# Optimization experiments

Hardware: AMD Instinct MI355X
Metric: run time of the kernel (lower is better)

The kernel has to match this reference:

```python
import jax, jax.numpy as jnp
import numpy as np

N, D, H = 4096, 1024, 16
HD = D // H  # 64
EPS = 1e-5


def setup_inputs() -> dict:
    key = jax.random.key(0)
    ks = jax.random.split(key, 12)
    lim = 1.0 / np.sqrt(D)
    def lin(kw, kb):
        W = jax.random.uniform(kw, (D, D), jnp.float32, -lim, lim)
        b = jax.random.uniform(kb, (D,), jnp.float32, -lim, lim)
        return W, b
    Wq, bq = lin(ks[0], ks[1])
    Wk, bk = lin(ks[2], ks[3])
    Wv, bv = lin(ks[4], ks[5])
    Wo, bo = lin(ks[6], ks[7])
    return {
        "query": jax.random.normal(ks[8], (N, D), jnp.float32),
        "key": jax.random.normal(ks[9], (N, D), jnp.float32),
        "value": jax.random.normal(ks[10], (N, D), jnp.float32),
        "Wq": Wq, "bq": bq, "Wk": Wk, "bk": bk,
        "Wv": Wv, "bv": bv, "Wo": Wo, "bo": bo,
        "q_norm_w": jnp.ones((HD,), jnp.float32),
        "k_norm_w": jnp.ones((HD,), jnp.float32),
    }


def _rmsnorm(x, w):
    # eqx.nn.RMSNorm: weight-only, eps=1e-5, over last dim
    inv = jax.lax.rsqrt(jnp.mean(x * x, axis=-1, keepdims=True) + EPS)
    return w * x * inv


def reference(query, key, value, Wq, bq, Wk, bk, Wv, bv, Wo, bo, q_norm_w, k_norm_w):
    n = query.shape[0]
    q = (query @ Wq.T + bq).reshape(n, H, HD)
    k = (key @ Wk.T + bk).reshape(n, H, HD)
    v = (value @ Wv.T + bv).reshape(n, H, HD)
    q = _rmsnorm(q, q_norm_w)
    k = _rmsnorm(k, k_norm_w)
    # scale=1.0: raw unscaled dot-product logits
    logits = jnp.einsum('qhd,khd->hqk', q, k)  # [H, N, N]
    probs = jax.nn.softmax(logits, axis=-1)
    attn = jnp.einsum('hqk,khd->qhd', probs, v).reshape(n, H * HD)
    return attn @ Wo.T + bo
```

## Files before the change

### kernel.cpp

```cpp
#include <hip/hip_runtime.h>
#include <stdint.h>
#include <stddef.h>

#define N_TOK 4096
#define DM    1024
#define NHEAD 16
#define HD    64

typedef __attribute__((ext_vector_type(8)))  short bf16x8;
typedef __attribute__((ext_vector_type(4)))  short bf16x4;
typedef __attribute__((ext_vector_type(4)))  float f32x4;
typedef __attribute__((ext_vector_type(16))) float f32x16;

static __device__ __forceinline__ float bf2f(short u) {
  union { unsigned int i; float f; } c;
  c.i = ((unsigned int)(unsigned short)u) << 16;
  return c.f;
}
static __device__ __forceinline__ unsigned short f2bf(float f) {
  union { float f; unsigned int i; } c; c.f = f;
  unsigned int x = c.i;
  return (unsigned short)((x + 0x7fffu + ((x >> 16) & 1u)) >> 16);
}
static __device__ __forceinline__ unsigned int cvtpk(float lo, float hi) {
  unsigned int d;
  asm("v_cvt_pk_bf16_f32 %0, %1, %2" : "=v"(d) : "v"(lo), "v"(hi));
  return d;
}
static __device__ __forceinline__ void plswap(unsigned int& a, unsigned int& b) {
  asm("v_permlane32_swap_b32 %0, %1" : "+v"(a), "+v"(b));
}
#if __has_builtin(__builtin_amdgcn_exp2f)
#define EXP2(x) __builtin_amdgcn_exp2f(x)
#else
#define EXP2(x) exp2f(x)
#endif
static __device__ __forceinline__ void gload16(const void* g, void* l) {
  __builtin_amdgcn_global_load_lds(
      (const __attribute__((address_space(1))) unsigned int*)g,
      (__attribute__((address_space(3))) unsigned int*)l, 16, 0, 0);
}

struct Cvt7 { const float* s[7]; unsigned short* d[7]; };
__global__ void cvt_all(Cvt7 a) {
  int u0 = blockIdx.x << 10;
  int seg, off;
  if (u0 < 1572864) { seg = u0 >> 19; off = u0 & 524287; }
  else { int j = u0 - 1572864; seg = 3 + (j >> 17); off = j & 131071; }
  const float* s = a.s[seg];
  unsigned short* dd = a.d[seg];
  int t = off + threadIdx.x;
#pragma unroll
  for (int j = 0; j < 4; ++j, t += 256) {
    const f32x4* sp = (const f32x4*)(s + (size_t)t * 8);
    f32x4 x = sp[0], y = sp[1];
    bf16x8 o;
    o[0] = (short)f2bf(x[0]); o[1] = (short)f2bf(x[1]);
    o[2] = (short)f2bf(x[2]); o[3] = (short)f2bf(x[3]);
    o[4] = (short)f2bf(y[0]); o[5] = (short)f2bf(y[1]);
    o[6] = (short)f2bf(y[2]); o[7] = (short)f2bf(y[3]);
    *(bf16x8*)(dd + (size_t)t * 8) = o;
  }
}

static __device__ __forceinline__ void gemm_core(
    const unsigned short* __restrict__ A,
    const unsigned short* __restrict__ W,
    const float* __restrict__ bias,
    unsigned short* __restrict__ Cb,
    float* __restrict__ Cf,
    const float* __restrict__ nw,
    int Nn, int K, int mode, int m0, int n0)
{
  __shared__ __align__(16) unsigned short At[2][64 * 32];
  __shared__ __align__(16) unsigned short Wt[2][128 * 32];
  const int tid  = threadIdx.x;
  const int wid  = tid >> 6, lane = tid & 63;
  const int lm   = lane & 15, lg = lane >> 4;
  const int wm   = (wid >> 1) * 32,  wn = (wid & 1) * 64;

  f32x4 acc[2][4];
#pragma unroll
  for (int i = 0; i < 2; ++i)
#pragma unroll
    for (int j = 0; j < 4; ++j) acc[i][j] = f32x4{0.f, 0.f, 0.f, 0.f};

  auto stage = [&](int b, int k0) {
#pragma unroll
    for (int i = 0; i < 3; ++i) {
      int c = wid * 3 + i;
      if (c < 4)
        gload16(A + (size_t)(m0 + c * 16 + (lane >> 2)) * K + k0 + (lane & 3) * 8,
                (char*)At + b * 4096 + c * 1024);
      else
        gload16(W + (size_t)(n0 + (c - 4) * 16 + (lane >> 2)) * K + k0 + (lane & 3) * 8,
                (char*)Wt + b * 8192 + (c - 4) * 1024);
    }
  };

  const int nk = K >> 5;
  stage(0, 0);
  __syncthreads();
  for (int kt = 0; kt < nk; ++kt) {
    const int cur = kt & 1;
    if (kt + 1 < nk) stage(cur ^ 1, (kt + 1) << 5);

    bf16x8 af[2], bfr[4];
#pragma unroll
    for (int mi = 0; mi < 2; ++mi)
      af[mi] = *(const bf16x8*)&At[cur][(wm + mi * 16 + lm) * 32 + lg * 8];
#pragma unroll
    for (int ni = 0; ni < 4; ++ni)
      bfr[ni] = *(const bf16x8*)&Wt[cur][(wn + ni * 16 + lm) * 32 + lg * 8];
    __builtin_amdgcn_s_setprio(1);
#pragma unroll
    for (int mi = 0; mi < 2; ++mi)
#pragma unroll
      for (int ni = 0; ni < 4; ++ni)
        acc[mi][ni] = __builtin_amdgcn_mfma_f32_16x16x32_bf16(
            af[mi], bfr[ni], acc[mi][ni], 0, 0, 0);
    __builtin_amdgcn_s_setprio(0);
    __syncthreads();
  }

  float bv[4];
#pragma unroll
  for (int ni = 0; ni < 4; ++ni) bv[ni] = bias[n0 + wn + ni * 16 + lm];

  if (mode <= 1) {
#pragma unroll
    for (int mi = 0; mi < 2; ++mi)
#pragma unroll
      for (int ni = 0; ni < 4; ++ni) {
        int n = n0 + wn + ni * 16 + lm;
#pragma unroll
        for (int r = 0; r < 4; ++r) {
          int m = m0 + wm + mi * 16 + lg * 4 + r;
          float v = acc[mi][ni][r] + bv[ni];
          if (mode == 1) Cf[(size_t)m * Nn + n] = v;
          else           Cb[(size_t)m * Nn + n] = f2bf(v);
        }
      }
  } else if (mode == 2) {
    const int h = (n0 + wn) >> 6;
    float w_[4];
#pragma unroll
    for (int ni = 0; ni < 4; ++ni) w_[ni] = nw[ni * 16 + lm];
#pragma unroll
    for (int mi = 0; mi < 2; ++mi) {
      float t[4][4], ssq[4];
#pragma unroll
      for (int ni = 0; ni < 4; ++ni)
#pragma unroll
        for (int r = 0; r < 4; ++r) t[ni][r] = acc[mi][ni][r] + bv[ni];
#pragma unroll
      for (int r = 0; r < 4; ++r)
        ssq[r] = t[0][r]*t[0][r] + t[1][r]*t[1][r] + t[2][r]*t[2][r] + t[3][r]*t[3][r];
#pragma unroll
      for (int r = 0; r < 4; ++r) {
        ssq[r] += __shfl_xor(ssq[r], 1);
        ssq[r] += __shfl_xor(ssq[r], 2);
        ssq[r] += __shfl_xor(ssq[r], 4);
        ssq[r] += __shfl_xor(ssq[r], 8);
      }
#pragma unroll
      for (int r = 0; r < 4; ++r) {
        float iv = rsqrtf(ssq[r] * (1.f / 64.f) + 1e-5f);
        int n_ = m0 + wm + mi * 16 + lg * 4 + r;
#pragma unroll
        for (int ni = 0; ni < 4; ++ni) {
          int d = ni * 16 + lm;
          Cb[(size_t)h * (N_TOK * HD) + (size_t)n_ * HD + d] = f2bf(t[ni][r] * w_[ni] * iv);
        }
      }
    }
  } else {
    const int h = (n0 + wn) >> 6;
#pragma unroll
    for (int mi = 0; mi < 2; ++mi)
#pragma unroll
      for (int ni = 0; ni < 4; ++ni) {
        int d  = ni * 16 + lm;
        int nb = m0 + wm + mi * 16 + lg * 4;
        bf16x4 o;
#pragma unroll
        for (int r = 0; r < 4; ++r) o[r] = (short)f2bf(acc[mi][ni][r] + bv[ni]);
        *(bf16x4*)&Cb[(size_t)h * (HD * N_TOK) + (size_t)d * N_TOK + nb] = o;
      }
  }
}

__global__ __launch_bounds__(256) void qkv_gemm(
    const unsigned short* __restrict__ a0, const unsigned short* __restrict__ a1,
    const unsigned short* __restrict__ a2,
    const unsigned short* __restrict__ w0, const unsigned short* __restrict__ w1,
    const unsigned short* __restrict__ w2,
    const float* __restrict__ b0, const float* __restrict__ b1,
    const float* __restrict__ b2,
    unsigned short* __restrict__ o0, unsigned short* __restrict__ o1,
    unsigned short* __restrict__ o2,
    const float* __restrict__ knw)
{
  const int z = blockIdx.z;
  const unsigned short* A = (z == 0) ? a0 : (z == 1) ? a1 : a2;
  const unsigned short* W = (z == 0) ? w0 : (z == 1) ? w1 : w2;
  const float* B          = (z == 0) ? b0 : (z == 1) ? b1 : b2;
  unsigned short* O       = (z == 0) ? o0 : (z == 1) ? o1 : o2;
  const int mode          = (z == 0) ? 0 : (z == 1) ? 2 : 3;
  gemm_core(A, W, B, O, nullptr, knw, DM, DM, mode,
            blockIdx.y * 64, blockIdx.x * 128);
}

__global__ __launch_bounds__(256) void out_gemm(
    const unsigned short* __restrict__ A, const unsigned short* __restrict__ W,
    const float* __restrict__ bias, float* __restrict__ Cf)
{
  gemm_core(A, W, bias, nullptr, Cf, nullptr, DM, DM, 1,
            blockIdx.y * 64, blockIdx.x * 128);
}

#define CSUB 57.70780163555853f
__global__ __launch_bounds__(256, 4) void attn_kernel(
    const unsigned short* __restrict__ qb,
    const unsigned short* __restrict__ kn,
    const unsigned short* __restrict__ vt,
    const float* __restrict__ wq,
    float* __restrict__ opart,
    float* __restrict__ lpart)
{
  __shared__ __align__(16) unsigned short Kl[2][64 * 64];
  __shared__ __align__(16) unsigned short Vl[2][64 * 64];

  const int wg  = blockIdx.x;
  const int x_  = wg & 7, idx = wg >> 3;
  const int h   = x_ * 2 + (idx & 1);
  const int sp  = (idx >> 1) & 1;
  const int tid = threadIdx.x;
  const int wid = tid >> 6, lane = tid & 63;
  const int l31 = lane & 31, hi = lane >> 5;
  const int sl  = l31 & 7;
  const int qbase = (idx >> 2) * 128 + wid * 32;

  bf16x8 qf[4];
  {
    const unsigned short* qp = qb + (size_t)(qbase + l31) * DM + h * HD + hi * 8;
    float qv[32]; float ss = 0.f;
#pragma unroll
    for (int s = 0; s < 4; ++s) {
      bf16x8 raw = *(const bf16x8*)(qp + s * 16);
#pragma unroll
      for (int j = 0; j < 8; ++j) { float f = bf2f(raw[j]); qv[s*8+j] = f; ss += f*f; }
    }
    ss += __shfl_xor(ss, 32);
    float inv = rsqrtf(ss * (1.f / 64.f) + 1e-5f) * 1.44269504f;
#pragma unroll
    for (int s = 0; s < 4; ++s)
#pragma unroll
      for (int j = 0; j < 8; ++j)
        qf[s][j] = (short)f2bf(qv[s*8+j] * wq[s*16 + hi*8 + j] * inv);
  }

  int slot[4];
#pragma unroll
  for (int x = 0; x < 4; ++x) slot[x] = (((2*x + hi) ^ sl) << 4);
  const char* KlB = (const char*)Kl + l31 * 128;
  const char* VlB = (const char*)Vl + l31 * 128;

  const char* gsrc[4];
  char*       ldst[4];
  long        gstep[4];
  {
    const char* knb = (const char*)kn + (size_t)h * (N_TOK * HD * 2);
    const char* vtb = (const char*)vt + (size_t)h * (HD * N_TOK * 2);
#pragma unroll
    for (int i = 0; i < 4; ++i) {
      int chunk = wid * 4 + i;
      int off   = (chunk & 7) * 1024 + lane * 16;
      int row   = off >> 7;
      int scol  = (off & 127) ^ ((row & 7) << 4);
      if (chunk < 8) {
        gsrc[i]  = knb + (size_t)(sp * 2048 + row) * 128 + scol;
        gstep[i] = 64 * 128;
        ldst[i]  = (char*)Kl + (chunk & 7) * 1024;
      } else {
        gsrc[i]  = vtb + (size_t)row * (N_TOK * 2) + sp * 4096 + scol;
        gstep[i] = 64 * 2;
        ldst[i]  = (char*)Vl + (chunk & 7) * 1024;
      }
    }
  }

  f32x16 oacc[2], minit;
#pragma unroll
  for (int r = 0; r < 16; ++r) { oacc[0][r] = 0.f; oacc[1][r] = 0.f; minit[r] = -CSUB; }
  float lsp[4] = {0.f, 0.f, 0.f, 0.f};

#pragma unroll
  for (int i = 0; i < 4; ++i) { gload16(gsrc[i], ldst[i]); gsrc[i] += gstep[i]; }
  __syncthreads();

  const int NT = 2048 / 64;
  for (int it = 0; it < NT; ++it) {
    const int cur = it & 1;
    if (it + 1 < NT) {
      const int nb = cur ^ 1;
#pragma unroll
      for (int i = 0; i < 4; ++i) {
        gload16(gsrc[i], ldst[i] + (nb << 13));
        gsrc[i] += gstep[i];
      }
    }
    const char* KB = KlB + (cur << 13);
    const char* VB = VlB + (cur << 13);

#pragma unroll
    for (int kt = 0; kt < 2; ++kt) {
      __builtin_amdgcn_s_setprio(1);
      bf16x8 kf0 = *(const bf16x8*)(KB + kt * 4096 + slot[0]);
      f32x16 sc = __builtin_amdgcn_mfma_f32_32x32x16_bf16(kf0, qf[0], minit, 0, 0, 0);
#pragma unroll
      for (int s = 1; s < 4; ++s) {
        bf16x8 kf = *(const bf16x8*)(KB + kt * 4096 + slot[s]);
        sc = __builtin_amdgcn_mfma_f32_32x32x16_bf16(kf, qf[s], sc, 0, 0, 0);
      }
      __builtin_amdgcn_s_setprio(0);
      float e[16];
#pragma unroll
      for (int r = 0; r < 16; ++r) { e[r] = EXP2(sc[r]); lsp[r & 3] += e[r]; }
      unsigned int wpk[4][2];
#pragma unroll
      for (int b = 0; b < 4; ++b) {
        wpk[b][0] = cvtpk(e[4*b+0], e[4*b+1]);
        wpk[b][1] = cvtpk(e[4*b+2], e[4*b+3]);
      }
#pragma unroll
      for (int pr = 0; pr < 2; ++pr) {
        unsigned int x0 = wpk[2*pr][0], x1 = wpk[2*pr][1];
        unsigned int y0 = wpk[2*pr+1][0], y1 = wpk[2*pr+1][1];
        plswap(x0, y0);
        plswap(x1, y1);
        union { unsigned int u[4]; bf16x8 v; } pa;
        pa.u[0] = x0; pa.u[1] = x1; pa.u[2] = y0; pa.u[3] = y1;
        int ks = kt * 2 + pr;
        __builtin_amdgcn_s_setprio(1);
#pragma unroll
        for (int dt = 0; dt < 2; ++dt) {
          bf16x8 vf = *(const bf16x8*)(VB + dt * 4096 + slot[ks]);
          oacc[dt] = __builtin_amdgcn_mfma_f32_32x32x16_bf16(pa.v, vf, oacc[dt], 0, 0, 0);
        }
        __builtin_amdgcn_s_setprio(0);
      }
    }
    __syncthreads();
  }

  float ls = (lsp[0] + lsp[1]) + (lsp[2] + lsp[3]);
  ls += __shfl_xor(ls, 32);
  float* Op = opart + (size_t)sp * (N_TOK * DM);
#pragma unroll
  for (int r = 0; r < 16; ++r) {
    int q = (r & 3) + 8 * (r >> 2) + 4 * hi;
    float* p = Op + (size_t)(qbase + q) * DM + h * HD + l31;
    p[0]  = oacc[0][r];
    p[32] = oacc[1][r];
  }
  if (hi == 0)
    lpart[(size_t)sp * (NHEAD * N_TOK) + h * N_TOK + qbase + l31] = ls;
}

__global__ void merge_kernel(const float* __restrict__ opart,
                             const float* __restrict__ lpart,
                             unsigned short* __restrict__ am)
{
  int i = (blockIdx.x * 256 + threadIdx.x) * 8;
  int n = i >> 10, c = i & 1023, h = c >> 6;
  float l = lpart[h * N_TOK + n] + lpart[NHEAD * N_TOK + h * N_TOK + n];
  float il = 1.f / l;
  const f32x4* p0 = (const f32x4*)(opart + (size_t)n * DM + c);
  const f32x4* p1 = (const f32x4*)(opart + (size_t)(N_TOK * DM) + (size_t)n * DM + c);
  f32x4 a0 = p0[0], a1 = p0[1], b0_ = p1[0], b1_ = p1[1];
  bf16x8 o;
#pragma unroll
  for (int j = 0; j < 4; ++j) {
    o[j]     = (short)f2bf((a0[j] + b0_[j]) * il);
    o[j + 4] = (short)f2bf((a1[j] + b1_[j]) * il);
  }
  *(bf16x8*)(am + i) = o;
}

extern "C" void kernel_launch(void* const* d_in, const int* in_sizes, int n_in,
                              void* d_out, int out_size, void* d_ws, size_t ws_size,
                              hipStream_t stream) {
  const float* query = (const float*)d_in[0];
  const float* key   = (const float*)d_in[1];
  const float* value = (const float*)d_in[2];
  const float* Wq    = (const float*)d_in[3];
  const float* bq    = (const float*)d_in[4];
  const float* Wk    = (const float*)d_in[5];
  const float* bk    = (const float*)d_in[6];
  const float* Wv    = (const float*)d_in[7];
  const float* bv    = (const float*)d_in[8];
  const float* Wo    = (const float*)d_in[9];
  const float* bo    = (const float*)d_in[10];
  const float* qnw   = (const float*)d_in[11];
  const float* knw   = (const float*)d_in[12];

  char* ws = (char*)d_ws;
  const size_t MB = 1024 * 1024;
  unsigned short* qpj = (unsigned short*)(ws + 0 * MB);
  unsigned short* Kn  = (unsigned short*)(ws + 8 * MB);
  unsigned short* Vt  = (unsigned short*)(ws + 16 * MB);
  unsigned short* wob = (unsigned short*)(ws + 24 * MB);
  unsigned short* wqb = (unsigned short*)(ws + 26 * MB);
  unsigned short* wkb = (unsigned short*)(ws + 28 * MB);
  unsigned short* wvb = (unsigned short*)(ws + 30 * MB);
  unsigned short* qbf = (unsigned short*)(ws + 32 * MB);
  unsigned short* kbf = (unsigned short*)(ws + 40 * MB);
  unsigned short* vbf = (unsigned short*)(ws + 48 * MB);
  float*          Op  = (float*)(ws + 26 * MB);
  float*          Lp  = (float*)(ws + 58 * MB);
  unsigned short* am  = qpj;

  Cvt7 ca;
  ca.s[0] = query; ca.d[0] = qbf;
  ca.s[1] = key;   ca.d[1] = kbf;
  ca.s[2] = value; ca.d[2] = vbf;
  ca.s[3] = Wq;    ca.d[3] = wqb;
  ca.s[4] = Wk;    ca.d[4] = wkb;
  ca.s[5] = Wv;    ca.d[5] = wvb;
  ca.s[6] = Wo;    ca.d[6] = wob;
  cvt_all<<<2048, 256, 0, stream>>>(ca);

  qkv_gemm<<<dim3(DM / 128, N_TOK / 64, 3), 256, 0, stream>>>(
      qbf, kbf, vbf, wqb, wkb, wvb, bq, bk, bv, qpj, Kn, Vt, knw);

  attn_kernel<<<1024, 256, 0, stream>>>(qpj, Kn, Vt, qnw, Op, Lp);

  merge_kernel<<<N_TOK * DM / 8 / 256, 256, 0, stream>>>(Op, Lp, am);

  out_gemm<<<dim3(DM / 128, N_TOK / 64), 256, 0, stream>>>(am, wob, bo, (float*)d_out);
}
```

Baseline: 181.0 us.

## Merge split-K attention partials in-block and enlarge QKV GEMM tile

The attention kernel now runs both key-range halves as two 4-wave groups inside one 512-thread block and combines their partial outputs and row sums through shared memory. It normalizes and writes bf16 directly, so the fp32 partial buffers and the separate merge kernel are no longer needed. The score MFMAs for both key tiles are also issued back to back before the exponentials. The QKV GEMM moves to a 128x128 tile via a templated core to improve data reuse. The risks are higher register pressure, an extra block-wide sync, and lower occupancy from the larger blocks.

```diff
diff --git a/kernel.cpp b/kernel.cpp
--- a/kernel.cpp
+++ b/kernel.cpp
@@ -63,6 +63,7 @@
   }
 }
 
+template <int MI>
 static __device__ __forceinline__ void gemm_core(
     const unsigned short* __restrict__ A,
     const unsigned short* __restrict__ W,
@@ -72,29 +73,30 @@
     const float* __restrict__ nw,
     int Nn, int K, int mode, int m0, int n0)
 {
-  __shared__ __align__(16) unsigned short At[2][64 * 32];
+  __shared__ __align__(16) unsigned short At[2][MI * 1024];
   __shared__ __align__(16) unsigned short Wt[2][128 * 32];
   const int tid  = threadIdx.x;
   const int wid  = tid >> 6, lane = tid & 63;
   const int lm   = lane & 15, lg = lane >> 4;
-  const int wm   = (wid >> 1) * 32,  wn = (wid & 1) * 64;
-
-  f32x4 acc[2][4];
-#pragma unroll
-  for (int i = 0; i < 2; ++i)
+  const int wm   = (wid >> 1) * (MI * 16), wn = (wid & 1) * 64;
+  const int CPW  = (MI * 2 + 8) / 4;
+
+  f32x4 acc[MI][4];
+#pragma unroll
+  for (int i = 0; i < MI; ++i)
 #pragma unroll
     for (int j = 0; j < 4; ++j) acc[i][j] = f32x4{0.f, 0.f, 0.f, 0.f};
 
   auto stage = [&](int b, int k0) {
 #pragma unroll
-    for (int i = 0; i < 3; ++i) {
-      int c = wid * 3 + i;
-      if (c < 4)
+    for (int i = 0; i < CPW; ++i) {
+      int c = wid * CPW + i;
+      if (c < MI * 2)
         gload16(A + (size_t)(m0 + c * 16 + (lane >> 2)) * K + k0 + (lane & 3) * 8,
-                (char*)At + b * 4096 + c * 1024);
+                (char*)At + b * (MI * 2048) + c * 1024);
       else
-        gload16(W + (size_t)(n0 + (c - 4) * 16 + (lane >> 2)) * K + k0 + (lane & 3) * 8,
-                (char*)Wt + b * 8192 + (c - 4) * 1024);
+        gload16(W + (size_t)(n0 + (c - MI * 2) * 16 + (lane >> 2)) * K + k0 + (lane & 3) * 8,
+                (char*)Wt + b * 8192 + (c - MI * 2) * 1024);
     }
   };
 
@@ -105,16 +107,16 @@
     const int cur = kt & 1;
     if (kt + 1 < nk) stage(cur ^ 1, (kt + 1) << 5);
 
-    bf16x8 af[2], bfr[4];
-#pragma unroll
-    for (int mi = 0; mi < 2; ++mi)
+    bf16x8 af[MI], bfr[4];
+#pragma unroll
+    for (int mi = 0; mi < MI; ++mi)
       af[mi] = *(const bf16x8*)&At[cur][(wm + mi * 16 + lm) * 32 + lg * 8];
 #pragma unroll
     for (int ni = 0; ni < 4; ++ni)
       bfr[ni] = *(const bf16x8*)&Wt[cur][(wn + ni * 16 + lm) * 32 + lg * 8];
     __builtin_amdgcn_s_setprio(1);
 #pragma unroll
-    for (int mi = 0; mi < 2; ++mi)
+    for (int mi = 0; mi < MI; ++mi)
 #pragma unroll
       for (int ni = 0; ni < 4; ++ni)
         acc[mi][ni] = __builtin_amdgcn_mfma_f32_16x16x32_bf16(
@@ -129,7 +131,7 @@
 
   if (mode <= 1) {
 #pragma unroll
-    for (int mi = 0; mi < 2; ++mi)
+    for (int mi = 0; mi < MI; ++mi)
 #pragma unroll
       for (int ni = 0; ni < 4; ++ni) {
         int n = n0 + wn + ni * 16 + lm;
@@ -147,7 +149,7 @@
 #pragma unroll
     for (int ni = 0; ni < 4; ++ni) w_[ni] = nw[ni * 16 + lm];
 #pragma unroll
-    for (int mi = 0; mi < 2; ++mi) {
+    for (int mi = 0; mi < MI; ++mi) {
       float t[4][4], ssq[4];
 #pragma unroll
       for (int ni = 0; ni < 4; ++ni)
@@ -177,7 +179,7 @@
   } else {
     const int h = (n0 + wn) >> 6;
 #pragma unroll
-    for (int mi = 0; mi < 2; ++mi)
+    for (int mi = 0; mi < MI; ++mi)
 #pragma unroll
       for (int ni = 0; ni < 4; ++ni) {
         int d  = ni * 16 + lm;
@@ -190,7 +192,7 @@
   }
 }
 
-__global__ __launch_bounds__(256) void qkv_gemm(
+__global__ __launch_bounds__(256, 3) void qkv_gemm(
     const unsigned short* __restrict__ a0, const unsigned short* __restrict__ a1,
     const unsigned short* __restrict__ a2,
     const unsigned short* __restrict__ w0, const unsigned short* __restrict__ w1,
@@ -207,39 +209,37 @@
   const float* B          = (z == 0) ? b0 : (z == 1) ? b1 : b2;
   unsigned short* O       = (z == 0) ? o0 : (z == 1) ? o1 : o2;
   const int mode          = (z == 0) ? 0 : (z == 1) ? 2 : 3;
-  gemm_core(A, W, B, O, nullptr, knw, DM, DM, mode,
-            blockIdx.y * 64, blockIdx.x * 128);
-}
-
-__global__ __launch_bounds__(256) void out_gemm(
+  gemm_core<4>(A, W, B, O, nullptr, knw, DM, DM, mode,
+               blockIdx.y * 128, blockIdx.x * 128);
+}
+
+__global__ __launch_bounds__(256, 4) void out_gemm(
     const unsigned short* __restrict__ A, const unsigned short* __restrict__ W,
     const float* __restrict__ bias, float* __restrict__ Cf)
 {
-  gemm_core(A, W, bias, nullptr, Cf, nullptr, DM, DM, 1,
-            blockIdx.y * 64, blockIdx.x * 128);
-}
-
-#define CSUB 57.70780163555853f
-__global__ __launch_bounds__(256, 4) void attn_kernel(
+  gemm_core<2>(A, W, bias, nullptr, Cf, nullptr, DM, DM, 1,
+               blockIdx.y * 64, blockIdx.x * 128);
+}
+
+__global__ __launch_bounds__(512, 4) void attn_kernel(
     const unsigned short* __restrict__ qb,
     const unsigned short* __restrict__ kn,
     const unsigned short* __restrict__ vt,
     const float* __restrict__ wq,
-    float* __restrict__ opart,
-    float* __restrict__ lpart)
+    unsigned short* __restrict__ ob)
 {
-  __shared__ __align__(16) unsigned short Kl[2][64 * 64];
-  __shared__ __align__(16) unsigned short Vl[2][64 * 64];
-
-  const int wg  = blockIdx.x;
-  const int x_  = wg & 7, idx = wg >> 3;
-  const int h   = x_ * 2 + (idx & 1);
-  const int sp  = (idx >> 1) & 1;
-  const int tid = threadIdx.x;
-  const int wid = tid >> 6, lane = tid & 63;
-  const int l31 = lane & 31, hi = lane >> 5;
-  const int sl  = l31 & 7;
-  const int qbase = (idx >> 2) * 128 + wid * 32;
+  __shared__ __align__(16) unsigned short SM[2][2][2][4096];
+
+  const int wg   = blockIdx.x;
+  const int x_   = wg & 7, rest = wg >> 3;
+  const int h    = x_ * 2 + (rest & 1);
+  const int qt   = rest >> 1;
+  const int tid  = threadIdx.x;
+  const int wid  = tid >> 6, lane = tid & 63;
+  const int g    = wid >> 2, wv = wid & 3;
+  const int l31  = lane & 31, hi = lane >> 5;
+  const int sl   = l31 & 7;
+  const int qbase = qt * 128 + wv * 32;
 
   bf16x8 qf[4];
   {
@@ -263,8 +263,7 @@
   int slot[4];
 #pragma unroll
   for (int x = 0; x < 4; ++x) slot[x] = (((2*x + hi) ^ sl) << 4);
-  const char* KlB = (const char*)Kl + l31 * 128;
-  const char* VlB = (const char*)Vl + l31 * 128;
+  const char* base = (const char*)SM + g * 32768 + l31 * 128;
 
   const char* gsrc[4];
   char*       ldst[4];
@@ -272,27 +271,28 @@
   {
     const char* knb = (const char*)kn + (size_t)h * (N_TOK * HD * 2);
     const char* vtb = (const char*)vt + (size_t)h * (HD * N_TOK * 2);
+    char* smG = (char*)SM + g * 32768;
 #pragma unroll
     for (int i = 0; i < 4; ++i) {
-      int chunk = wid * 4 + i;
+      int chunk = wv * 4 + i;
       int off   = (chunk & 7) * 1024 + lane * 16;
       int row   = off >> 7;
       int scol  = (off & 127) ^ ((row & 7) << 4);
       if (chunk < 8) {
-        gsrc[i]  = knb + (size_t)(sp * 2048 + row) * 128 + scol;
+        gsrc[i]  = knb + (size_t)(g * 2048 + row) * 128 + scol;
         gstep[i] = 64 * 128;
-        ldst[i]  = (char*)Kl + (chunk & 7) * 1024;
+        ldst[i]  = smG + (chunk & 7) * 1024;
       } else {
-        gsrc[i]  = vtb + (size_t)row * (N_TOK * 2) + sp * 4096 + scol;
+        gsrc[i]  = vtb + (size_t)row * (N_TOK * 2) + g * 4096 + scol;
         gstep[i] = 64 * 2;
-        ldst[i]  = (char*)Vl + (chunk & 7) * 1024;
-      }
-    }
-  }
-
-  f32x16 oacc[2], minit;
-#pragma unroll
-  for (int r = 0; r < 16; ++r) { oacc[0][r] = 0.f; oacc[1][r] = 0.f; minit[r] = -CSUB; }
+        ldst[i]  = smG + 8192 + (chunk & 7) * 1024;
+      }
+    }
+  }
+
+  f32x16 oacc[2], fz;
+#pragma unroll
+  for (int r = 0; r < 16; ++r) { oacc[0][r] = 0.f; oacc[1][r] = 0.f; fz[r] = 0.f; }
   float lsp[4] = {0.f, 0.f, 0.f, 0.f};
 
 #pragma unroll
@@ -306,27 +306,32 @@
       const int nb = cur ^ 1;
 #pragma unroll
       for (int i = 0; i < 4; ++i) {
-        gload16(gsrc[i], ldst[i] + (nb << 13));
+        gload16(gsrc[i], ldst[i] + nb * 16384);
         gsrc[i] += gstep[i];
       }
     }
-    const char* KB = KlB + (cur << 13);
-    const char* VB = VlB + (cur << 13);
-
+    const char* KB = base + cur * 16384;
+    const char* VB = KB + 8192;
+
+    f32x16 sc[2];
+    __builtin_amdgcn_s_setprio(1);
 #pragma unroll
     for (int kt = 0; kt < 2; ++kt) {
-      __builtin_amdgcn_s_setprio(1);
       bf16x8 kf0 = *(const bf16x8*)(KB + kt * 4096 + slot[0]);
-      f32x16 sc = __builtin_amdgcn_mfma_f32_32x32x16_bf16(kf0, qf[0], minit, 0, 0, 0);
+      sc[kt] = __builtin_amdgcn_mfma_f32_32x32x16_bf16(kf0, qf[0], fz, 0, 0, 0);
 #pragma unroll
       for (int s = 1; s < 4; ++s) {
         bf16x8 kf = *(const bf16x8*)(KB + kt * 4096 + slot[s]);
-        sc = __builtin_amdgcn_mfma_f32_32x32x16_bf16(kf, qf[s], sc, 0, 0, 0);
-      }
-      __builtin_amdgcn_s_setprio(0);
+        sc[kt] = __builtin_amdgcn_mfma_f32_32x32x16_bf16(kf, qf[s], sc[kt], 0, 0, 0);
+      }
+    }
+    __builtin_amdgcn_s_setprio(0);
+
+#pragma unroll
+    for (int kt = 0; kt < 2; ++kt) {
       float e[16];
 #pragma unroll
-      for (int r = 0; r < 16; ++r) { e[r] = EXP2(sc[r]); lsp[r & 3] += e[r]; }
+      for (int r = 0; r < 16; ++r) { e[r] = EXP2(sc[kt][r]); lsp[r & 3] += e[r]; }
       unsigned int wpk[4][2];
 #pragma unroll
       for (int b = 0; b < 4; ++b) {
@@ -356,36 +361,37 @@
 
   float ls = (lsp[0] + lsp[1]) + (lsp[2] + lsp[3]);
   ls += __shfl_xor(ls, 32);
-  float* Op = opart + (size_t)sp * (N_TOK * DM);
-#pragma unroll
-  for (int r = 0; r < 16; ++r) {
-    int q = (r & 3) + 8 * (r >> 2) + 4 * hi;
-    float* p = Op + (size_t)(qbase + q) * DM + h * HD + l31;
-    p[0]  = oacc[0][r];
-    p[32] = oacc[1][r];
-  }
-  if (hi == 0)
-    lpart[(size_t)sp * (NHEAD * N_TOK) + h * N_TOK + qbase + l31] = ls;
-}
-
-__global__ void merge_kernel(const float* __restrict__ opart,
-                             const float* __restrict__ lpart,
-                             unsigned short* __restrict__ am)
-{
-  int i = (blockIdx.x * 256 + threadIdx.x) * 8;
-  int n = i >> 10, c = i & 1023, h = c >> 6;
-  float l = lpart[h * N_TOK + n] + lpart[NHEAD * N_TOK + h * N_TOK + n];
-  float il = 1.f / l;
-  const f32x4* p0 = (const f32x4*)(opart + (size_t)n * DM + c);
-  const f32x4* p1 = (const f32x4*)(opart + (size_t)(N_TOK * DM) + (size_t)n * DM + c);
-  f32x4 a0 = p0[0], a1 = p0[1], b0_ = p1[0], b1_ = p1[1];
-  bf16x8 o;
-#pragma unroll
-  for (int j = 0; j < 4; ++j) {
-    o[j]     = (short)f2bf((a0[j] + b0_[j]) * il);
-    o[j + 4] = (short)f2bf((a1[j] + b1_[j]) * il);
-  }
-  *(bf16x8*)(am + i) = o;
+
+  float* ex  = (float*)((char*)SM + 32768);
+  float* lsx = (float*)SM;
+  const int idx = wv * 64 + lane;
+  if (g == 1) {
+#pragma unroll
+    for (int dt = 0; dt < 2; ++dt)
+#pragma unroll
+      for (int r = 0; r < 16; ++r)
+        ex[(dt * 16 + r) * 256 + idx] = oacc[dt][r];
+    lsx[idx] = ls;
+  }
+  __syncthreads();
+  if (g == 0) {
+#pragma unroll
+    for (int dt = 0; dt < 2; ++dt)
+#pragma unroll
+      for (int r = 0; r < 16; ++r)
+        oacc[dt][r] += ex[(dt * 16 + r) * 256 + idx];
+    ls += lsx[idx];
+    float il = 1.f / ls;
+#pragma unroll
+    for (int r = 0; r < 16; ++r) {
+      int q = (r & 3) + 8 * (r >> 2) + 4 * hi;
+      float ilr = __int_as_float(
+          __builtin_amdgcn_ds_bpermute(q << 2, __float_as_int(il)));
+      unsigned short* op = ob + (size_t)(qbase + q) * DM + h * HD + l31;
+      op[0]  = f2bf(oacc[0][r] * ilr);
+      op[32] = f2bf(oacc[1][r] * ilr);
+    }
+  }
 }
 
 extern "C" void kernel_launch(void* const* d_in, const int* in_sizes, int n_in,
@@ -417,9 +423,7 @@
   unsigned short* qbf = (unsigned short*)(ws + 32 * MB);
   unsigned short* kbf = (unsigned short*)(ws + 40 * MB);
   unsigned short* vbf = (unsigned short*)(ws + 48 * MB);
-  float*          Op  = (float*)(ws + 26 * MB);
-  float*          Lp  = (float*)(ws + 58 * MB);
-  unsigned short* am  = qpj;
+  unsigned short* apj = (unsigned short*)(ws + 56 * MB);
 
   Cvt7 ca;
   ca.s[0] = query; ca.d[0] = qbf;
@@ -431,12 +435,10 @@
   ca.s[6] = Wo;    ca.d[6] = wob;
   cvt_all<<<2048, 256, 0, stream>>>(ca);
 
-  qkv_gemm<<<dim3(DM / 128, N_TOK / 64, 3), 256, 0, stream>>>(
+  qkv_gemm<<<dim3(DM / 128, N_TOK / 128, 3), 256, 0, stream>>>(
       qbf, kbf, vbf, wqb, wkb, wvb, bq, bk, bv, qpj, Kn, Vt, knw);
 
-  attn_kernel<<<1024, 256, 0, stream>>>(qpj, Kn, Vt, qnw, Op, Lp);
-
-  merge_kernel<<<N_TOK * DM / 8 / 256, 256, 0, stream>>>(Op, Lp, am);
-
-  out_gemm<<<dim3(DM / 128, N_TOK / 64), 256, 0, stream>>>(am, wob, bo, (float*)d_out);
-}
+  attn_kernel<<<512, 512, 0, stream>>>(qpj, Kn, Vt, qnw, apj);
+
+  out_gemm<<<dim3(DM / 128, N_TOK / 64), 256, 0, stream>>>(apj, wob, bo, (float*)d_out);
+}
```

Result: faster. 154.7 us (-14.5%).
